# Optimization experiments

Hardware: AMD Instinct MI355X
Metric: run time of the kernel (lower is better)

## Reference

```python
import jax, jax.numpy as jnp
import numpy as np

EPS = 1e-5
TOP_K = 50

def _layernorm(h, g, b):
    mu = jnp.mean(h, axis=-1, keepdims=True)
    var = jnp.mean((h - mu) ** 2, axis=-1, keepdims=True)
    return (h - mu) * jax.lax.rsqrt(var + EPS) * g + b

def setup_inputs() -> dict:
    key = jax.random.key(0)
    ks = jax.random.split(key, 8)
    B, D, E = 16384, 384, 2048
    return {
        "x": jax.random.normal(ks[0], (B, D), jnp.float32),
        "We": jax.random.normal(ks[1], (D, E), jnp.float32) * 0.05,
        "be": jax.random.normal(ks[2], (E,), jnp.float32) * 0.01,
        "g1": jnp.ones((E,), jnp.float32),
        "b1": jnp.zeros((E,), jnp.float32),
        "Wd": jax.random.normal(ks[3], (E, D), jnp.float32) * 0.02,
        "bd": jax.random.normal(ks[4], (D,), jnp.float32) * 0.01,
        "Wb": jax.random.normal(ks[5], (E, D), jnp.float32) * 0.02,
        "bb": jax.random.normal(ks[6], (D,), jnp.float32) * 0.01,
        "g2": jnp.ones((D,), jnp.float32),
        "b2": jnp.zeros((D,), jnp.float32),
    }

def reference(x, We, be, g1, b1, Wd, bd, Wb, bb, g2, b2):
    # encoder: Linear -> LayerNorm -> ReLU
    h = jax.nn.relu(_layernorm(x @ We + be, g1, b1))  # [B, E]
    # top-k sparsification: zero all but top-50 per row (scatter mask, matches torch)
    _, idx = jax.lax.top_k(h, TOP_K)                  # [B, K]
    rows = jnp.arange(h.shape[0])[:, None]
    mask = jnp.zeros_like(h).at[rows, idx].set(1.0)
    sparse = h * mask                                 # [B, E]
    recon = sparse @ Wd + bd                          # [B, D]
    separated = _layernorm(sparse @ Wb + bb, g2, b2)  # [B, D]
    return recon, sparse, separated
```

## Files before the change

kernel.cpp:

```cpp
#include <hip/hip_runtime.h>
#include <hip/hip_bf16.h>
#include <stdint.h>

#define B_D   384
#define B_E   2048
#define TOPK  50
#define LN_EPS 1e-5f
#define NKS   18
#define NKP   12
#define FIX_WINDOW 2e-4f

typedef short bf16x8 __attribute__((ext_vector_type(8)));
typedef float f32x4  __attribute__((ext_vector_type(4)));

__device__ __forceinline__ float wave_sum_f(float v) {
#pragma unroll
    for (int d = 1; d < 64; d <<= 1) v += __shfl_xor(v, d, 64);
    return v;
}
__device__ __forceinline__ int wave_sum_i(int v) {
#pragma unroll
    for (int d = 1; d < 64; d <<= 1) v += __shfl_xor(v, d, 64);
    return v;
}
__device__ __forceinline__ float wave_max_f(float v) {
#pragma unroll
    for (int d = 1; d < 64; d <<= 1) v = fmaxf(v, __shfl_xor(v, d, 64));
    return v;
}

__device__ __forceinline__ ushort f2bf_hi(float v) {
    __hip_bfloat16 b = __float2bfloat16(v);
    return *(ushort*)&b;
}
__device__ __forceinline__ ushort f2bf_lo(float v) {
    __hip_bfloat16 b = __float2bfloat16(v);
    float rem = v - __bfloat162float(b);
    __hip_bfloat16 l = __float2bfloat16(rem);
    return *(ushort*)&l;
}

__device__ __forceinline__ void llds16(const void* g, void* l) {
    __builtin_amdgcn_global_load_lds((const __attribute__((address_space(1))) void*)g,
                                     (__attribute__((address_space(3))) void*)l, 16, 0, 0);
}

__global__ __launch_bounds__(256) void pack_A(const float* __restrict__ x, ushort* __restrict__ Ap,
                                              int* __restrict__ cntr)
{
    const int ks = blockIdx.x, mt = blockIdx.y, t = threadIdx.x;
    if (cntr && t == 0 && ks == 0 && mt == 0) *cntr = 0;
#pragma unroll
    for (int q = 0; q < 8; ++q) {
        const int s = q * 256 + t;
        const int m = s & 255, kg = s >> 8;
        const int kp = ks * 64 + kg * 8;
        const int hi = (kp < 384);
        const int ksrc = hi ? kp : kp - 384;
        const float* src = x + (size_t)(mt * 256 + m) * B_D + ksrc;
        float4 v0 = *(const float4*)src;
        float4 v1 = *(const float4*)(src + 4);
        float vv[8] = {v0.x, v0.y, v0.z, v0.w, v1.x, v1.y, v1.z, v1.w};
        ushort o[8];
#pragma unroll
        for (int e = 0; e < 8; ++e)
            o[e] = hi ? f2bf_hi(vv[e]) : f2bf_lo(vv[e]);
        *(uint4*)(Ap + ((size_t)(mt * NKP + ks) * 2048 + s) * 8) = *(uint4*)o;
    }
}

__global__ __launch_bounds__(256) void pack_B(const float* __restrict__ We, ushort* __restrict__ Bp)
{
    const int ks = blockIdx.x, nt = blockIdx.y, t = threadIdx.x;
#pragma unroll
    for (int q = 0; q < 8; ++q) {
        const int s = q * 256 + t;
        const int nl = s & 255, kg = s >> 8;
        const int kp = ks * 64 + kg * 8;
        const int hi = (kp < 384);
        const int ksrc = hi ? kp : kp - 384;
        const int ng = nt * 256 + nl;
        ushort o[8];
#pragma unroll
        for (int e = 0; e < 8; ++e) {
            float v = We[(size_t)(ksrc + e) * B_E + ng];
            o[e] = hi ? f2bf_hi(v) : f2bf_lo(v);
        }
        *(uint4*)(Bp + ((size_t)(nt * NKP + ks) * 2048 + s) * 8) = *(uint4*)o;
    }
}

__global__ __launch_bounds__(128) void pack_W(
    const float* __restrict__ Wd, const float* __restrict__ Wb, uint* __restrict__ Wp)
{
    const int e = blockIdx.x, t = threadIdx.x;
#pragma unroll
    for (int j = 0; j < 3; ++j) {
        const int c = t + 128 * j;
        const ushort d = f2bf_hi(Wd[(size_t)e * B_D + c]);
        const ushort b = f2bf_hi(Wb[(size_t)e * B_D + c]);
        Wp[(size_t)e * B_D + c] = ((uint)b << 16) | (uint)d;
    }
}

__global__ __launch_bounds__(512, 2) void enc_mfma256(
    const ushort* __restrict__ Ap, const ushort* __restrict__ Bp,
    const float* __restrict__ be, float* __restrict__ y)
{
    __shared__ __align__(16) ushort As[2][16384];
    __shared__ __align__(16) ushort Bs[2][16384];
    const int t = threadIdx.x, lane = t & 63, w = t >> 6;
    const int wr = w >> 2, wc = w & 3;
    const int gid = blockIdx.x;
    const int swz = (gid & 7) * 64 + (gid >> 3);
    const int nt = swz & 7, mt = swz >> 3;
    const ushort* gA = Ap + (size_t)mt * NKP * 16384;
    const ushort* gB = Bp + (size_t)nt * NKP * 16384;

    f32x4 acc[8][4];
#pragma unroll
    for (int i = 0; i < 8; ++i)
#pragma unroll
        for (int j = 0; j < 4; ++j)
#pragma unroll
            for (int r = 0; r < 4; ++r) acc[i][j][r] = 0.f;

    const int l15 = lane & 15, l4 = lane >> 4;

#define STAGE256(ls_, buf_)                                                     \
    {                                                                           \
        const int lsv = (ls_);                                                  \
        const int ksA = (lsv < 6) ? lsv : lsv - 6;                              \
        const int ksB = (lsv < 12) ? lsv : lsv - 12;                            \
        const ushort* a_src = gA + (size_t)ksA * 16384 + t * 8;                 \
        const ushort* b_src = gB + (size_t)ksB * 16384 + t * 8;                 \
        _Pragma("unroll")                                                       \
        for (int q = 0; q < 4; ++q) {                                           \
            llds16(a_src + q * 4096, &As[buf_][t * 8 + q * 4096]);              \
            llds16(b_src + q * 4096, &Bs[buf_][t * 8 + q * 4096]);              \
        }                                                                       \
    }

    STAGE256(0, 0);
    __syncthreads();

    for (int ls = 0; ls < NKS; ++ls) {
        const int cur = ls & 1;
        if (ls + 1 < NKS) STAGE256(ls + 1, cur ^ 1);
#pragma unroll
        for (int ko = 0; ko < 2; ++ko) {
            const int kg = ko * 4 + l4;
            bf16x8 af[8], bfr[4];
#pragma unroll
            for (int i = 0; i < 8; ++i)
                af[i] = *(const bf16x8*)&As[cur][(kg * 256 + wr * 128 + i * 16 + l15) * 8];
#pragma unroll
            for (int j = 0; j < 4; ++j)
                bfr[j] = *(const bf16x8*)&Bs[cur][(kg * 256 + wc * 64 + j * 16 + l15) * 8];
#pragma unroll
            for (int i = 0; i < 8; ++i)
#pragma unroll
                for (int j = 0; j < 4; ++j)
                    acc[i][j] = __builtin_amdgcn_mfma_f32_16x16x32_bf16(af[i], bfr[j], acc[i][j], 0, 0, 0);
        }
        if (ls + 1 < NKS) __syncthreads();
    }
#undef STAGE256

    float bev[4];
#pragma unroll
    for (int j = 0; j < 4; ++j) bev[j] = be[nt * 256 + wc * 64 + j * 16 + l15];
#pragma unroll
    for (int i = 0; i < 8; ++i)
#pragma unroll
        for (int j = 0; j < 4; ++j)
#pragma unroll
            for (int r = 0; r < 4; ++r) {
                const int row = mt * 256 + wr * 128 + i * 16 + l4 * 4 + r;
                const int col = nt * 256 + wc * 64 + j * 16 + l15;
                y[(size_t)row * B_E + col] = acc[i][j][r] + bev[j];
            }
}

__global__ __launch_bounds__(256) void enc_gemm_f32(
    const float* __restrict__ x, const float* __restrict__ We,
    const float* __restrict__ be, float* __restrict__ y)
{
    __shared__ float As[8][128];
    __shared__ float Bs[8][128];
    const int t  = threadIdx.x;
    const int m0 = blockIdx.y * 128;
    const int n0 = blockIdx.x * 128;
    const int tx = t & 15, ty = t >> 4;
    const int la_m = t >> 1, la_k = (t & 1) * 4;
    const int lb_k = t >> 5, lb_c = (t & 31) * 4;

    float acc[8][8];
#pragma unroll
    for (int i = 0; i < 8; ++i)
#pragma unroll
        for (int j = 0; j < 8; ++j) acc[i][j] = 0.f;

    for (int k0 = 0; k0 < B_D; k0 += 8) {
        float4 a = *(const float4*)&x[(size_t)(m0 + la_m) * B_D + k0 + la_k];
        float4 b = *(const float4*)&We[(size_t)(k0 + lb_k) * B_E + n0 + lb_c];
        __syncthreads();
        As[la_k + 0][la_m] = a.x;
        As[la_k + 1][la_m] = a.y;
        As[la_k + 2][la_m] = a.z;
        As[la_k + 3][la_m] = a.w;
        *(float4*)&Bs[lb_k][lb_c] = b;
        __syncthreads();
#pragma unroll
        for (int kk = 0; kk < 8; ++kk) {
            float4 a0 = *(const float4*)&As[kk][ty * 4];
            float4 a1 = *(const float4*)&As[kk][ty * 4 + 64];
            float4 b0 = *(const float4*)&Bs[kk][tx * 4];
            float4 b1 = *(const float4*)&Bs[kk][tx * 4 + 64];
            float av[8] = {a0.x,a0.y,a0.z,a0.w,a1.x,a1.y,a1.z,a1.w};
            float bv[8] = {b0.x,b0.y,b0.z,b0.w,b1.x,b1.y,b1.z,b1.w};
#pragma unroll
            for (int i = 0; i < 8; ++i)
#pragma unroll
                for (int j = 0; j < 8; ++j)
                    acc[i][j] = fmaf(av[i], bv[j], acc[i][j]);
        }
    }
    float4 beL = *(const float4*)&be[n0 + tx * 4];
    float4 beH = *(const float4*)&be[n0 + 64 + tx * 4];
    float bl[8] = {beL.x,beL.y,beL.z,beL.w,beH.x,beH.y,beH.z,beH.w};
#pragma unroll
    for (int i = 0; i < 8; ++i) {
        int row = m0 + ty * 4 + (i & 3) + (i >> 2) * 64;
        float4 o0 = {acc[i][0]+bl[0], acc[i][1]+bl[1], acc[i][2]+bl[2], acc[i][3]+bl[3]};
        float4 o1 = {acc[i][4]+bl[4], acc[i][5]+bl[5], acc[i][6]+bl[6], acc[i][7]+bl[7]};
        *(float4*)&y[(size_t)row * B_E + n0 + tx * 4]      = o0;
        *(float4*)&y[(size_t)row * B_E + n0 + 64 + tx * 4] = o1;
    }
}

__device__ __forceinline__ int ln_topk_row(
    float (&h)[32], int lane, const float* __restrict__ g1, const float* __restrict__ b1,
    float* __restrict__ row, int* __restrict__ IwR, float* __restrict__ VwR,
    float* __restrict__ ldsv, int* __restrict__ ldsi)
{
    float s = 0.f;
#pragma unroll
    for (int j = 0; j < 32; ++j) s += h[j];
    s = wave_sum_f(s);
    const float mu = s * (1.f / B_E);
    float ss = 0.f;
#pragma unroll
    for (int j = 0; j < 32; ++j) { float d = h[j] - mu; ss += d * d; }
    ss = wave_sum_f(ss);
    const float rstd = rsqrtf(ss * (1.f / B_E) + LN_EPS);
#pragma unroll
    for (int q = 0; q < 8; ++q) {
        float4 g  = *(const float4*)&g1[q * 256 + lane * 4];
        float4 bb = *(const float4*)&b1[q * 256 + lane * 4];
        float gg[4]  = {g.x,g.y,g.z,g.w};
        float bbv[4] = {bb.x,bb.y,bb.z,bb.w};
#pragma unroll
        for (int i = 0; i < 4; ++i) {
            int j = q*4+i;
            h[j] = fmaxf(fmaf((h[j] - mu) * rstd, gg[i], bbv[i]), 0.f);
        }
    }
    float mx = h[0];
#pragma unroll
    for (int j = 1; j < 32; ++j) mx = fmaxf(mx, h[j]);
    mx = wave_max_f(mx);

    float vlo = 0.f, vhi = __uint_as_float(__float_as_uint(mx) + 1u);
    int cl = 2048;
    bool window = false;
    for (int it = 0; it < 20; ++it) {
        float mid = 0.5f * (vlo + vhi);
        if (it == 0 && 2.2f > vlo && 2.2f < vhi) mid = 2.2f;
        if (!(mid > vlo && mid < vhi)) break;
        int c = 0;
#pragma unroll
        for (int j = 0; j < 32; ++j)
            c += (int)__popcll(__ballot(h[j] >= mid));
        if (c >= TOPK) { vlo = mid; cl = c; if (c <= 64) { window = true; break; } }
        else vhi = mid;
    }
    unsigned lo = __float_as_uint(vlo);
    if (!window) {
        unsigned hi = __float_as_uint(vhi);
        while (hi - lo > 1u) {
            const unsigned mid = lo + ((hi - lo) >> 1);
            const float mf = __uint_as_float(mid);
            int c = 0;
#pragma unroll
            for (int j = 0; j < 32; ++j)
                c += (int)__popcll(__ballot(h[j] >= mf));
            if (c >= TOPK) { lo = mid; cl = c; if (c <= 64) break; }
            else hi = mid;
        }
    }
    const float T0 = __uint_as_float(lo);

    unsigned selmask = 0u;
    int flag = 0;
    bool fastSel = (cl <= 64 && T0 > 0.f);

    if (fastSel) {
        ldsv[lane] = -1.f;
        ldsi[lane] = 1 << 20;
        asm volatile("s_waitcnt lgkmcnt(0)" ::: "memory");
        int base = 0;
#pragma unroll
        for (int j = 0; j < 32; ++j) {
            const bool p = (h[j] >= T0);
            const unsigned long long m = __ballot(p);
            if (p) {
                const int pos = base + (int)__popcll(m & ((1ull << lane) - 1ull));
                ldsv[pos] = h[j];
                ldsi[pos] = (j >> 2) * 256 + lane * 4 + (j & 3);
            }
            base += (int)__popcll(m);
        }
        asm volatile("s_waitcnt lgkmcnt(0)" ::: "memory");
        float sv = ldsv[lane];
        int   si = ldsi[lane];
#pragma unroll
        for (int k = 2; k <= 64; k <<= 1) {
#pragma unroll
            for (int jj = k >> 1; jj > 0; jj >>= 1) {
                const float ov = __shfl_xor(sv, jj, 64);
                const int   oi = __shfl_xor(si, jj, 64);
                const bool dirUp = ((lane & k) == 0);
                const bool lower = ((lane & jj) == 0);
                const bool mineBefore = (sv > ov) || (sv == ov && si < oi);
                const bool keep = (lower == dirUp) ? mineBefore : !mineBefore;
                if (!keep) { sv = ov; si = oi; }
            }
        }
        const float T    = __shfl(sv, TOPK - 1, 64);
        const int   idxT = __shfl(si, TOPK - 1, 64);
        float v51;
        if (cl > TOPK) {
            v51 = __shfl(sv, TOPK, 64);
        } else {
            float bb = -1.f;
#pragma unroll
            for (int j = 0; j < 32; ++j) bb = (h[j] < T0) ? fmaxf(bb, h[j]) : bb;
            v51 = wave_max_f(bb);
        }
        flag = (T - v51 < FIX_WINDOW) ? 1 : 0;
#pragma unroll
        for (int j = 0; j < 32; ++j) {
            const int e = (j >> 2) * 256 + lane * 4 + (j & 3);
            if (h[j] > T || (h[j] == T && e <= idxT)) selmask |= (1u << j);
        }
        if (lane < TOPK) { IwR[lane] = si; VwR[lane] = sv; }
    } else {
        const float T = T0;
        int cgt = 0, ceq = 0;
        float below = -1.f;
#pragma unroll
        for (int j = 0; j < 32; ++j) {
            cgt += (h[j] > T); ceq += (h[j] == T);
            if (h[j] < T) below = fmaxf(below, h[j]);
        }
        const int cgt_t = wave_sum_i(cgt);
        const int ceq_t = wave_sum_i(ceq);
        below = wave_max_f(below);
        const int need = TOPK - cgt_t;

        if (cgt_t + ceq_t == TOPK) {
#pragma unroll
            for (int j = 0; j < 32; ++j) if (h[j] >= T) selmask |= (1u << j);
        } else {
            int base = 0;
            for (int q = 0; q < 8; ++q) {
                int tc = 0;
#pragma unroll
                for (int i = 0; i < 4; ++i) tc += (h[q*4+i] == T);
                int ip = tc;
#pragma unroll
                for (int d = 1; d < 64; d <<= 1) {
                    int o = __shfl_up(ip, d, 64);
                    if (lane >= d) ip += o;
                }
                int rk  = base + ip - tc;
                int tot = __shfl(ip, 63, 64);
#pragma unroll
                for (int i = 0; i < 4; ++i) {
                    int j = q*4+i;
                    if (h[j] > T) selmask |= (1u << j);
                    else if (h[j] == T) { if (rk < need) selmask |= (1u << j); rk++; }
                }
                base += tot;
            }
        }
        if (T > 0.f) {
            if (cgt_t + ceq_t != TOPK && ceq_t > need) flag = 1;
            else if (T - below < FIX_WINDOW) flag = 1;
        }
        const int myc = __popc(selmask);
        int ip = myc;
#pragma unroll
        for (int d = 1; d < 64; d <<= 1) {
            int o = __shfl_up(ip, d, 64);
            if (lane >= d) ip += o;
        }
        int pos = ip - myc;
        for (int j = 0; j < 32; ++j) {
            if ((selmask >> j) & 1u) {
                int e = (j >> 2) * 256 + lane * 4 + (j & 3);
                IwR[pos] = e;
                VwR[pos] = h[j];
                pos++;
            }
        }
    }

#pragma unroll
    for (int q = 0; q < 8; ++q) {
        float4 o;
        o.x = ((selmask >> (q*4+0)) & 1u) ? h[q*4+0] : 0.f;
        o.y = ((selmask >> (q*4+1)) & 1u) ? h[q*4+1] : 0.f;
        o.z = ((selmask >> (q*4+2)) & 1u) ? h[q*4+2] : 0.f;
        o.w = ((selmask >> (q*4+3)) & 1u) ? h[q*4+3] : 0.f;
        *(float4*)&row[q * 256 + lane * 4] = o;
    }
    return flag;
}

__global__ __launch_bounds__(256) void ln_relu_topk_k(
    float* __restrict__ y, const float* __restrict__ g1, const float* __restrict__ b1,
    int* __restrict__ Iw, float* __restrict__ Vw,
    int* __restrict__ flags, int* __restrict__ rowlist, int* __restrict__ cntr)
{
    __shared__ float ldsv[4][64];
    __shared__ int   ldsi[4][64];
    const int lane = threadIdx.x & 63;
    const int w = threadIdx.x >> 6;
    const int r = blockIdx.x * 4 + w;
    float* row = y + (size_t)r * B_E;
    float h[32];
#pragma unroll
    for (int q = 0; q < 8; ++q) {
        float4 v = *(const float4*)&row[q * 256 + lane * 4];
        h[q*4+0] = v.x; h[q*4+1] = v.y; h[q*4+2] = v.z; h[q*4+3] = v.w;
    }
    int flag = ln_topk_row(h, lane, g1, b1, row, Iw + r * TOPK, Vw + r * TOPK,
                           ldsv[w], ldsi[w]);
    if (flags && lane == 0) {
        flags[r] = flag;
        if (flag) {
            int p = atomicAdd(cntr, 1);
            rowlist[p] = r;
        }
    }
}

__global__ __launch_bounds__(256) void fixup_recompute(
    const float* __restrict__ x, const float* __restrict__ We, const float* __restrict__ be,
    float* __restrict__ y, const int* __restrict__ rowlist, const int* __restrict__ cntr)
{
    const int nflag = *cntr;
    const int rb = blockIdx.y * 8;
    if (rb >= nflag) return;
    const int nact = min(nflag - rb, 8);
    const int t = threadIdx.x;

    __shared__ float xs[8][B_D];
    __shared__ int   rIdx[8];
    if (t < 8) rIdx[t] = (t < nact) ? rowlist[rb + t] : -1;
    __syncthreads();
#pragma unroll
    for (int i = 0; i < 8; ++i) {
        if (i < nact) {
            const float* src = x + (size_t)rIdx[i] * B_D;
            for (int j = t; j < B_D; j += 256) xs[i][j] = src[j];
        } else {
            for (int j = t; j < B_D; j += 256) xs[i][j] = 0.f;
        }
    }
    __syncthreads();

    const int c = blockIdx.x * 256 + t;
    const float bc = be[c];
    float acc[8];
#pragma unroll
    for (int i = 0; i < 8; ++i) acc[i] = bc;
#pragma unroll 4
    for (int k = 0; k < B_D; ++k) {
        const float w = We[(size_t)k * B_E + c];
#pragma unroll
        for (int i = 0; i < 8; ++i) acc[i] = fmaf(xs[i][k], w, acc[i]);
    }
#pragma unroll
    for (int i = 0; i < 8; ++i)
        if (i < nact) y[(size_t)rIdx[i] * B_E + c] = acc[i];
}

__global__ __launch_bounds__(256) void fixup_select(
    float* __restrict__ y, const float* __restrict__ g1, const float* __restrict__ b1,
    int* __restrict__ Iw, float* __restrict__ Vw, const int* __restrict__ flags)
{
    __shared__ float ldsv[4][64];
    __shared__ int   ldsi[4][64];
    const int w = threadIdx.x >> 6;
    const int r = blockIdx.x * 4 + w;
    if (!flags[r]) return;
    const int lane = threadIdx.x & 63;
    float* row = y + (size_t)r * B_E;
    float h[32];
#pragma unroll
    for (int q = 0; q < 8; ++q) {
        float4 v = *(const float4*)&row[q * 256 + lane * 4];
        h[q*4+0] = v.x; h[q*4+1] = v.y; h[q*4+2] = v.z; h[q*4+3] = v.w;
    }
    ln_topk_row(h, lane, g1, b1, row, Iw + r * TOPK, Vw + r * TOPK,
                ldsv[w], ldsi[w]);
}

__global__ __launch_bounds__(128) void decode_packed(
    const int* __restrict__ Iw, const float* __restrict__ Vw,
    const uint* __restrict__ Wp, const float* __restrict__ bd,
    const float* __restrict__ bbias, const float* __restrict__ g2,
    const float* __restrict__ b2, float* __restrict__ recon, float* __restrict__ sep)
{
    __shared__ int   sI[TOPK];
    __shared__ float sV[TOPK];
    __shared__ float red[2];
    const int r = blockIdx.x, t = threadIdx.x;
    if (t < TOPK) { sI[t] = Iw[r * TOPK + t]; sV[t] = Vw[r * TOPK + t]; }
    __syncthreads();
    float ad[3], ab[3];
#pragma unroll
    for (int j = 0; j < 3; ++j) { ad[j] = bd[t + 128*j]; ab[j] = bbias[t + 128*j]; }
#pragma unroll 2
    for (int i = 0; i < TOPK; ++i) {
        const int   idx = sI[i];
        const float v   = sV[i];
        const uint* wp  = Wp + (size_t)idx * B_D;
#pragma unroll
        for (int j = 0; j < 3; ++j) {
            const uint u = wp[t + 128*j];
            const float wd = __uint_as_float(u << 16);
            const float wb = __uint_as_float(u & 0xFFFF0000u);
            ad[j] = fmaf(v, wd, ad[j]);
            ab[j] = fmaf(v, wb, ab[j]);
        }
    }
#pragma unroll
    for (int j = 0; j < 3; ++j) recon[(size_t)r * B_D + t + 128*j] = ad[j];
    float s = ab[0] + ab[1] + ab[2];
    s = wave_sum_f(s);
    if ((t & 63) == 0) red[t >> 6] = s;
    __syncthreads();
    const float mu = (red[0] + red[1]) * (1.f / B_D);
    __syncthreads();
    float ss = 0.f;
#pragma unroll
    for (int j = 0; j < 3; ++j) { float d = ab[j] - mu; ss += d * d; }
    ss = wave_sum_f(ss);
    if ((t & 63) == 0) red[t >> 6] = ss;
    __syncthreads();
    const float rstd = rsqrtf((red[0] + red[1]) * (1.f / B_D) + LN_EPS);
#pragma unroll
    for (int j = 0; j < 3; ++j) {
        int c = t + 128*j;
        sep[(size_t)r * B_D + c] = fmaf((ab[j] - mu) * rstd, g2[c], b2[c]);
    }
}

__global__ __launch_bounds__(128) void decode_f32(
    const int* __restrict__ Iw, const float* __restrict__ Vw,
    const float* __restrict__ Wd, const float* __restrict__ bd,
    const float* __restrict__ Wb, const float* __restrict__ bbias,
    const float* __restrict__ g2, const float* __restrict__ b2,
    float* __restrict__ recon, float* __restrict__ sep)
{
    __shared__ int   sI[TOPK];
    __shared__ float sV[TOPK];
    __shared__ float red[2];
    const int r = blockIdx.x, t = threadIdx.x;
    if (t < TOPK) { sI[t] = Iw[r * TOPK + t]; sV[t] = Vw[r * TOPK + t]; }
    __syncthreads();
    float ad[3], ab[3];
#pragma unroll
    for (int j = 0; j < 3; ++j) { ad[j] = bd[t + 128*j]; ab[j] = bbias[t + 128*j]; }
#pragma unroll 2
    for (int i = 0; i < TOPK; ++i) {
        const int   idx = sI[i];
        const float v   = sV[i];
        const float* wd = Wd + (size_t)idx * B_D;
        const float* wb = Wb + (size_t)idx * B_D;
#pragma unroll
        for (int j = 0; j < 3; ++j) {
            ad[j] = fmaf(v, wd[t + 128*j], ad[j]);
            ab[j] = fmaf(v, wb[t + 128*j], ab[j]);
        }
    }
#pragma unroll
    for (int j = 0; j < 3; ++j) recon[(size_t)r * B_D + t + 128*j] = ad[j];
    float s = ab[0] + ab[1] + ab[2];
    s = wave_sum_f(s);
    if ((t & 63) == 0) red[t >> 6] = s;
    __syncthreads();
    const float mu = (red[0] + red[1]) * (1.f / B_D);
    __syncthreads();
    float ss = 0.f;
#pragma unroll
    for (int j = 0; j < 3; ++j) { float d = ab[j] - mu; ss += d * d; }
    ss = wave_sum_f(ss);
    if ((t & 63) == 0) red[t >> 6] = ss;
    __syncthreads();
    const float rstd = rsqrtf((red[0] + red[1]) * (1.f / B_D) + LN_EPS);
#pragma unroll
    for (int j = 0; j < 3; ++j) {
        int c = t + 128*j;
        sep[(size_t)r * B_D + c] = fmaf((ab[j] - mu) * rstd, g2[c], b2[c]);
    }
}

extern "C" void kernel_launch(void* const* d_in, const int* in_sizes, int n_in,
                              void* d_out, int out_size, void* d_ws, size_t ws_size,
                              hipStream_t stream)
{
    const float* x  = (const float*)d_in[0];
    const float* We = (const float*)d_in[1];
    const float* be = (const float*)d_in[2];
    const float* g1 = (const float*)d_in[3];
    const float* b1 = (const float*)d_in[4];
    const float* Wd = (const float*)d_in[5];
    const float* bd = (const float*)d_in[6];
    const float* Wb = (const float*)d_in[7];
    const float* bb = (const float*)d_in[8];
    const float* g2 = (const float*)d_in[9];
    const float* b2 = (const float*)d_in[10];

    const int Brows = in_sizes[0] / B_D;
    float* recon  = (float*)d_out;
    float* sparse = recon + (size_t)Brows * B_D;
    float* sep    = sparse + (size_t)Brows * B_E;

    char* ws = (char*)d_ws;
    int*   Iw      = (int*)ws;
    float* Vw      = (float*)(ws + 3276800);
    int*   flags   = (int*)(ws + 6553600);
    int*   rowlist = (int*)(ws + 6619136);
    int*   cntr    = (int*)(ws + 6684672);
    const size_t apOff = 6688768;
    const size_t bpOff = apOff + (size_t)64 * NKP * 2048 * 16;
    const size_t need  = bpOff + (size_t)8 * NKP * 2048 * 16;

    if (ws_size >= need) {
        ushort* Ap = (ushort*)(ws + apOff);
        ushort* Bp = (ushort*)(ws + bpOff);
        uint*   Wp = (uint*)(ws + apOff);
        pack_A<<<dim3(NKP, 64), dim3(256), 0, stream>>>(x, Ap, cntr);
        pack_B<<<dim3(NKP, 8),  dim3(256), 0, stream>>>(We, Bp);
        enc_mfma256<<<dim3(512), dim3(512), 0, stream>>>(Ap, Bp, be, sparse);
        pack_W<<<dim3(B_E), dim3(128), 0, stream>>>(Wd, Wb, Wp);
        ln_relu_topk_k<<<dim3(Brows / 4), dim3(256), 0, stream>>>(sparse, g1, b1, Iw, Vw, flags, rowlist, cntr);
        fixup_recompute<<<dim3(8, Brows / 8), dim3(256), 0, stream>>>(x, We, be, sparse, rowlist, cntr);
        fixup_select<<<dim3(Brows / 4), dim3(256), 0, stream>>>(sparse, g1, b1, Iw, Vw, flags);
        decode_packed<<<dim3(Brows), dim3(128), 0, stream>>>(Iw, Vw, Wp, bd, bb, g2, b2, recon, sep);
    } else {
        enc_gemm_f32<<<dim3(16, 128), dim3(256), 0, stream>>>(x, We, be, sparse);
        ln_relu_topk_k<<<dim3(Brows / 4), dim3(256), 0, stream>>>(sparse, g1, b1, Iw, Vw, nullptr, nullptr, nullptr);
        decode_f32<<<dim3(Brows), dim3(128), 0, stream>>>(Iw, Vw, Wd, bd, Wb, bb, g2, b2, recon, sep);
    }
}
```

Baseline: 287.7 us.

## Merge packing kernels and fuse fixup recompute with reselection into one persistent kernel

Combines pack_A and pack_B into a single launch and folds the Wd/Wb bf16 packing into the top-k kernel as extra blocks. The separate fixup_recompute and fixup_select kernels become one persistent fixup kernel. It recomputes flagged rows in fp32 into shared memory and reruns LN/top-k directly, removing the per-row flags array and the full-grid select pass. This cuts launch count and removes the wide grid of mostly-idle fixup blocks, at the cost of a 128-block fixup kernel with heavy shared-memory and register use.

New measurement: 332.1 us. 1.15x slower.

```diff
diff --git a/kernel.cpp b/kernel.cpp
--- a/kernel.cpp
+++ b/kernel.cpp
@@ -45,61 +45,49 @@
                                      (__attribute__((address_space(3))) void*)l, 16, 0, 0);
 }
 
-__global__ __launch_bounds__(256) void pack_A(const float* __restrict__ x, ushort* __restrict__ Ap,
-                                              int* __restrict__ cntr)
-{
-    const int ks = blockIdx.x, mt = blockIdx.y, t = threadIdx.x;
-    if (cntr && t == 0 && ks == 0 && mt == 0) *cntr = 0;
-#pragma unroll
-    for (int q = 0; q < 8; ++q) {
-        const int s = q * 256 + t;
-        const int m = s & 255, kg = s >> 8;
-        const int kp = ks * 64 + kg * 8;
-        const int hi = (kp < 384);
-        const int ksrc = hi ? kp : kp - 384;
-        const float* src = x + (size_t)(mt * 256 + m) * B_D + ksrc;
-        float4 v0 = *(const float4*)src;
-        float4 v1 = *(const float4*)(src + 4);
-        float vv[8] = {v0.x, v0.y, v0.z, v0.w, v1.x, v1.y, v1.z, v1.w};
-        ushort o[8];
-#pragma unroll
-        for (int e = 0; e < 8; ++e)
-            o[e] = hi ? f2bf_hi(vv[e]) : f2bf_lo(vv[e]);
-        *(uint4*)(Ap + ((size_t)(mt * NKP + ks) * 2048 + s) * 8) = *(uint4*)o;
-    }
-}
-
-__global__ __launch_bounds__(256) void pack_B(const float* __restrict__ We, ushort* __restrict__ Bp)
-{
-    const int ks = blockIdx.x, nt = blockIdx.y, t = threadIdx.x;
-#pragma unroll
-    for (int q = 0; q < 8; ++q) {
-        const int s = q * 256 + t;
-        const int nl = s & 255, kg = s >> 8;
-        const int kp = ks * 64 + kg * 8;
-        const int hi = (kp < 384);
-        const int ksrc = hi ? kp : kp - 384;
-        const int ng = nt * 256 + nl;
-        ushort o[8];
-#pragma unroll
-        for (int e = 0; e < 8; ++e) {
-            float v = We[(size_t)(ksrc + e) * B_E + ng];
-            o[e] = hi ? f2bf_hi(v) : f2bf_lo(v);
-        }
-        *(uint4*)(Bp + ((size_t)(nt * NKP + ks) * 2048 + s) * 8) = *(uint4*)o;
-    }
-}
-
-__global__ __launch_bounds__(128) void pack_W(
-    const float* __restrict__ Wd, const float* __restrict__ Wb, uint* __restrict__ Wp)
-{
-    const int e = blockIdx.x, t = threadIdx.x;
-#pragma unroll
-    for (int j = 0; j < 3; ++j) {
-        const int c = t + 128 * j;
-        const ushort d = f2bf_hi(Wd[(size_t)e * B_D + c]);
-        const ushort b = f2bf_hi(Wb[(size_t)e * B_D + c]);
-        Wp[(size_t)e * B_D + c] = ((uint)b << 16) | (uint)d;
+__global__ __launch_bounds__(256) void pack_AB(
+    const float* __restrict__ x, const float* __restrict__ We,
+    ushort* __restrict__ Ap, ushort* __restrict__ Bp, int* __restrict__ cntr)
+{
+    const int ks = blockIdx.x, yb = blockIdx.y, t = threadIdx.x;
+    if (cntr && t == 0 && ks == 0 && yb == 0) *cntr = 0;
+    if (yb < 64) {
+        const int mt = yb;
+#pragma unroll
+        for (int q = 0; q < 8; ++q) {
+            const int s = q * 256 + t;
+            const int m = s & 255, kg = s >> 8;
+            const int kp = ks * 64 + kg * 8;
+            const int hi = (kp < 384);
+            const int ksrc = hi ? kp : kp - 384;
+            const float* src = x + (size_t)(mt * 256 + m) * B_D + ksrc;
+            float4 v0 = *(const float4*)src;
+            float4 v1 = *(const float4*)(src + 4);
+            float vv[8] = {v0.x, v0.y, v0.z, v0.w, v1.x, v1.y, v1.z, v1.w};
+            ushort o[8];
+#pragma unroll
+            for (int e = 0; e < 8; ++e)
+                o[e] = hi ? f2bf_hi(vv[e]) : f2bf_lo(vv[e]);
+            *(uint4*)(Ap + ((size_t)(mt * NKP + ks) * 2048 + s) * 8) = *(uint4*)o;
+        }
+    } else {
+        const int nt = yb - 64;
+#pragma unroll
+        for (int q = 0; q < 8; ++q) {
+            const int s = q * 256 + t;
+            const int nl = s & 255, kg = s >> 8;
+            const int kp = ks * 64 + kg * 8;
+            const int hi = (kp < 384);
+            const int ksrc = hi ? kp : kp - 384;
+            const int ng = nt * 256 + nl;
+            ushort o[8];
+#pragma unroll
+            for (int e = 0; e < 8; ++e) {
+                float v = We[(size_t)(ksrc + e) * B_E + ng];
+                o[e] = hi ? f2bf_hi(v) : f2bf_lo(v);
+            }
+            *(uint4*)(Bp + ((size_t)(nt * NKP + ks) * 2048 + s) * 8) = *(uint4*)o;
+        }
     }
 }
 
@@ -429,10 +417,223 @@
     return flag;
 }
 
-__global__ __launch_bounds__(256) void ln_relu_topk_k(
+__global__ __launch_bounds__(256) void topk_packW(
     float* __restrict__ y, const float* __restrict__ g1, const float* __restrict__ b1,
     int* __restrict__ Iw, float* __restrict__ Vw,
-    int* __restrict__ flags, int* __restrict__ rowlist, int* __restrict__ cntr)
+    int* __restrict__ rowlist, int* __restrict__ cntr,
+    const float* __restrict__ Wd, const float* __restrict__ Wb, uint* __restrict__ Wp,
+    int nTopk)
+{
+    __shared__ float ldsv[4][64];
+    __shared__ int   ldsi[4][64];
+    const int bid = blockIdx.x;
+    const int t = threadIdx.x;
+    if (bid >= nTopk) {
+        const int e = (bid - nTopk) * 2 + (t >> 7);
+        const int tt = t & 127;
+#pragma unroll
+        for (int j = 0; j < 3; ++j) {
+            const int c = tt + 128 * j;
+            const ushort d = f2bf_hi(Wd[(size_t)e * B_D + c]);
+            const ushort b = f2bf_hi(Wb[(size_t)e * B_D + c]);
+            Wp[(size_t)e * B_D + c] = ((uint)b << 16) | (uint)d;
+        }
+        return;
+    }
+    const int lane = t & 63;
+    const int w = t >> 6;
+    const int r = bid * 4 + w;
+    float* row = y + (size_t)r * B_E;
+    float h[32];
+#pragma unroll
+    for (int q = 0; q < 8; ++q) {
+        float4 v = *(const float4*)&row[q * 256 + lane * 4];
+        h[q*4+0] = v.x; h[q*4+1] = v.y; h[q*4+2] = v.z; h[q*4+3] = v.w;
+    }
+    int flag = ln_topk_row(h, lane, g1, b1, row, Iw + r * TOPK, Vw + r * TOPK,
+                           ldsv[w], ldsi[w]);
+    if (rowlist && lane == 0 && flag) {
+        int p = atomicAdd(cntr, 1);
+        rowlist[p] = r;
+    }
+}
+
+__global__ __launch_bounds__(256) void fixup_fused(
+    const float* __restrict__ x, const float* __restrict__ We, const float* __restrict__ be,
+    const float* __restrict__ g1, const float* __restrict__ b1,
+    float* __restrict__ y, int* __restrict__ Iw, float* __restrict__ Vw,
+    const int* __restrict__ rowlist, const int* __restrict__ cntr)
+{
+    const int nflag = *cntr;
+    __shared__ float xs[8][B_D];
+    __shared__ float hy[8][B_E];
+    __shared__ float ldsv[4][64];
+    __shared__ int   ldsi[4][64];
+    __shared__ int   rIdx[8];
+    const int t = threadIdx.x;
+    const int w = t >> 6, lane = t & 63;
+
+    for (int rb = blockIdx.x * 8; rb < nflag; rb += gridDim.x * 8) {
+        const int nact = min(nflag - rb, 8);
+        __syncthreads();
+        if (t < 8) rIdx[t] = (t < nact) ? rowlist[rb + t] : -1;
+        __syncthreads();
+#pragma unroll
+        for (int i = 0; i < 8; ++i) {
+            if (i < nact) {
+                const float* src = x + (size_t)rIdx[i] * B_D;
+                for (int j = t; j < B_D; j += 256) xs[i][j] = src[j];
+            } else {
+                for (int j = t; j < B_D; j += 256) xs[i][j] = 0.f;
+            }
+        }
+        __syncthreads();
+
+        float bev[8];
+#pragma unroll
+        for (int jj = 0; jj < 8; ++jj) bev[jj] = be[t + 256 * jj];
+        float acc[8][8];
+#pragma unroll
+        for (int i = 0; i < 8; ++i)
+#pragma unroll
+            for (int jj = 0; jj < 8; ++jj) acc[i][jj] = bev[jj];
+#pragma unroll 2
+        for (int k = 0; k < B_D; ++k) {
+            const float* wr = We + (size_t)k * B_E;
+            float w8[8];
+#pragma unroll
+            for (int jj = 0; jj < 8; ++jj) w8[jj] = wr[t + 256 * jj];
+#pragma unroll
+            for (int i = 0; i < 8; ++i) {
+                const float xv = xs[i][k];
+#pragma unroll
+                for (int jj = 0; jj < 8; ++jj) acc[i][jj] = fmaf(xv, w8[jj], acc[i][jj]);
+            }
+        }
+#pragma unroll
+        for (int i = 0; i < 8; ++i)
+#pragma unroll
+            for (int jj = 0; jj < 8; ++jj) hy[i][t + 256 * jj] = acc[i][jj];
+        __syncthreads();
+
+        for (int ii = w; ii < nact; ii += 4) {
+            const int r = rIdx[ii];
+            float h[32];
+#pragma unroll
+            for (int q = 0; q < 8; ++q) {
+                float4 v = *(const float4*)&hy[ii][q * 256 + lane * 4];
+                h[q*4+0] = v.x; h[q*4+1] = v.y; h[q*4+2] = v.z; h[q*4+3] = v.w;
+            }
+            ln_topk_row(h, lane, g1, b1, y + (size_t)r * B_E,
+                        Iw + r * TOPK, Vw + r * TOPK, ldsv[w], ldsi[w]);
+        }
+    }
+}
+
+__global__ __launch_bounds__(128) void decode_packed(
+    const int* __restrict__ Iw, const float* __restrict__ Vw,
+    const uint* __restrict__ Wp, const float* __restrict__ bd,
+    const float* __restrict__ bbias, const float* __restrict__ g2,
+    const float* __restrict__ b2, float* __restrict__ recon, float* __restrict__ sep)
+{
+    __shared__ int   sI[TOPK];
+    __shared__ float sV[TOPK];
+    __shared__ float red[2];
+    const int r = blockIdx.x, t = threadIdx.x;
+    if (t < TOPK) { sI[t] = Iw[r * TOPK + t]; sV[t] = Vw[r * TOPK + t]; }
+    __syncthreads();
+    float ad[3], ab[3];
+#pragma unroll
+    for (int j = 0; j < 3; ++j) { ad[j] = bd[t + 128*j]; ab[j] = bbias[t + 128*j]; }
+#pragma unroll 2
+    for (int i = 0; i < TOPK; ++i) {
+        const int   idx = sI[i];
+        const float v   = sV[i];
+        const uint* wp  = Wp + (size_t)idx * B_D;
+#pragma unroll
+        for (int j = 0; j < 3; ++j) {
+            const uint u = wp[t + 128*j];
+            const float wd = __uint_as_float(u << 16);
+            const float wb = __uint_as_float(u & 0xFFFF0000u);
+            ad[j] = fmaf(v, wd, ad[j]);
+            ab[j] = fmaf(v, wb, ab[j]);
+        }
+    }
+#pragma unroll
+    for (int j = 0; j < 3; ++j) recon[(size_t)r * B_D + t + 128*j] = ad[j];
+    float s = ab[0] + ab[1] + ab[2];
+    s = wave_sum_f(s);
+    if ((t & 63) == 0) red[t >> 6] = s;
+    __syncthreads();
+    const float mu = (red[0] + red[1]) * (1.f / B_D);
+    __syncthreads();
+    float ss = 0.f;
+#pragma unroll
+    for (int j = 0; j < 3; ++j) { float d = ab[j] - mu; ss += d * d; }
+    ss = wave_sum_f(ss);
+    if ((t & 63) == 0) red[t >> 6] = ss;
+    __syncthreads();
+    const float rstd = rsqrtf((red[0] + red[1]) * (1.f / B_D) + LN_EPS);
+#pragma unroll
+    for (int j = 0; j < 3; ++j) {
+        int c = t + 128*j;
+        sep[(size_t)r * B_D + c] = fmaf((ab[j] - mu) * rstd, g2[c], b2[c]);
+    }
+}
+
+__global__ __launch_bounds__(128) void decode_f32(
+    const int* __restrict__ Iw, const float* __restrict__ Vw,
+    const float* __restrict__ Wd, const float* __restrict__ bd,
+    const float* __restrict__ Wb, const float* __restrict__ bbias,
+    const float* __restrict__ g2, const float* __restrict__ b2,
+    float* __restrict__ recon, float* __restrict__ sep)
+{
+    __shared__ int   sI[TOPK];
+    __shared__ float sV[TOPK];
+    __shared__ float red[2];
+    const int r = blockIdx.x, t = threadIdx.x;
+    if (t < TOPK) { sI[t] = Iw[r * TOPK + t]; sV[t] = Vw[r * TOPK + t]; }
+    __syncthreads();
+    float ad[3], ab[3];
+#pragma unroll
+    for (int j = 0; j < 3; ++j) { ad[j] = bd[t + 128*j]; ab[j] = bbias[t + 128*j]; }
+#pragma unroll 2
+    for (int i = 0; i < TOPK; ++i) {
+        const int   idx = sI[i];
+        const float v   = sV[i];
+        const float* wd = Wd + (size_t)idx * B_D;
+        const float* wb = Wb + (size_t)idx * B_D;
+#pragma unroll
+        for (int j = 0; j < 3; ++j) {
+            ad[j] = fmaf(v, wd[t + 128*j], ad[j]);
+            ab[j] = fmaf(v, wb[t + 128*j], ab[j]);
+        }
+    }
+#pragma unroll
+    for (int j = 0; j < 3; ++j) recon[(size_t)r * B_D + t + 128*j] = ad[j];
+    float s = ab[0] + ab[1] + ab[2];
+    s = wave_sum_f(s);
+    if ((t & 63) == 0) red[t >> 6] = s;
+    __syncthreads();
+    const float mu = (red[0] + red[1]) * (1.f / B_D);
+    __syncthreads();
+    float ss = 0.f;
+#pragma unroll
+    for (int j = 0; j < 3; ++j) { float d = ab[j] - mu; ss += d * d; }
+    ss = wave_sum_f(ss);
+    if ((t & 63) == 0) red[t >> 6] = ss;
+    __syncthreads();
+    const float rstd = rsqrtf((red[0] + red[1]) * (1.f / B_D) + LN_EPS);
+#pragma unroll
+    for (int j = 0; j < 3; ++j) {
+        int c = t + 128*j;
+        sep[(size_t)r * B_D + c] = fmaf((ab[j] - mu) * rstd, g2[c], b2[c]);
+    }
+}
+
+__global__ __launch_bounds__(256) void topk_only(
+    float* __restrict__ y, const float* __restrict__ g1, const float* __restrict__ b1,
+    int* __restrict__ Iw, float* __restrict__ Vw)
 {
     __shared__ float ldsv[4][64];
     __shared__ int   ldsi[4][64];
@@ -446,178 +647,7 @@
         float4 v = *(const float4*)&row[q * 256 + lane * 4];
         h[q*4+0] = v.x; h[q*4+1] = v.y; h[q*4+2] = v.z; h[q*4+3] = v.w;
     }
-    int flag = ln_topk_row(h, lane, g1, b1, row, Iw + r * TOPK, Vw + r * TOPK,
-                           ldsv[w], ldsi[w]);
-    if (flags && lane == 0) {
-        flags[r] = flag;
-        if (flag) {
-            int p = atomicAdd(cntr, 1);
-            rowlist[p] = r;
-        }
-    }
-}
-
-__global__ __launch_bounds__(256) void fixup_recompute(
-    const float* __restrict__ x, const float* __restrict__ We, const float* __restrict__ be,
-    float* __restrict__ y, const int* __restrict__ rowlist, const int* __restrict__ cntr)
-{
-    const int nflag = *cntr;
-    const int rb = blockIdx.y * 8;
-    if (rb >= nflag) return;
-    const int nact = min(nflag - rb, 8);
-    const int t = threadIdx.x;
-
-    __shared__ float xs[8][B_D];
-    __shared__ int   rIdx[8];
-    if (t < 8) rIdx[t] = (t < nact) ? rowlist[rb + t] : -1;
-    __syncthreads();
-#pragma unroll
-    for (int i = 0; i < 8; ++i) {
-        if (i < nact) {
-            const float* src = x + (size_t)rIdx[i] * B_D;
-            for (int j = t; j < B_D; j += 256) xs[i][j] = src[j];
-        } else {
-            for (int j = t; j < B_D; j += 256) xs[i][j] = 0.f;
-        }
-    }
-    __syncthreads();
-
-    const int c = blockIdx.x * 256 + t;
-    const float bc = be[c];
-    float acc[8];
-#pragma unroll
-    for (int i = 0; i < 8; ++i) acc[i] = bc;
-#pragma unroll 4
-    for (int k = 0; k < B_D; ++k) {
-        const float w = We[(size_t)k * B_E + c];
-#pragma unroll
-        for (int i = 0; i < 8; ++i) acc[i] = fmaf(xs[i][k], w, acc[i]);
-    }
-#pragma unroll
-    for (int i = 0; i < 8; ++i)
-        if (i < nact) y[(size_t)rIdx[i] * B_E + c] = acc[i];
-}
-
-__global__ __launch_bounds__(256) void fixup_select(
-    float* __restrict__ y, const float* __restrict__ g1, const float* __restrict__ b1,
-    int* __restrict__ Iw, float* __restrict__ Vw, const int* __restrict__ flags)
-{
-    __shared__ float ldsv[4][64];
-    __shared__ int   ldsi[4][64];
-    const int w = threadIdx.x >> 6;
-    const int r = blockIdx.x * 4 + w;
-    if (!flags[r]) return;
-    const int lane = threadIdx.x & 63;
-    float* row = y + (size_t)r * B_E;
-    float h[32];
-#pragma unroll
-    for (int q = 0; q < 8; ++q) {
-        float4 v = *(const float4*)&row[q * 256 + lane * 4];
-        h[q*4+0] = v.x; h[q*4+1] = v.y; h[q*4+2] = v.z; h[q*4+3] = v.w;
-    }
-    ln_topk_row(h, lane, g1, b1, row, Iw + r * TOPK, Vw + r * TOPK,
-                ldsv[w], ldsi[w]);
-}
-
-__global__ __launch_bounds__(128) void decode_packed(
-    const int* __restrict__ Iw, const float* __restrict__ Vw,
-    const uint* __restrict__ Wp, const float* __restrict__ bd,
-    const float* __restrict__ bbias, const float* __restrict__ g2,
-    const float* __restrict__ b2, float* __restrict__ recon, float* __restrict__ sep)
-{
-    __shared__ int   sI[TOPK];
-    __shared__ float sV[TOPK];
-    __shared__ float red[2];
-    const int r = blockIdx.x, t = threadIdx.x;
-    if (t < TOPK) { sI[t] = Iw[r * TOPK + t]; sV[t] = Vw[r * TOPK + t]; }
-    __syncthreads();
-    float ad[3], ab[3];
-#pragma unroll
-    for (int j = 0; j < 3; ++j) { ad[j] = bd[t + 128*j]; ab[j] = bbias[t + 128*j]; }
-#pragma unroll 2
-    for (int i = 0; i < TOPK; ++i) {
-        const int   idx = sI[i];
-        const float v   = sV[i];
-        const uint* wp  = Wp + (size_t)idx * B_D;
-#pragma unroll
-        for (int j = 0; j < 3; ++j) {
-            const uint u = wp[t + 128*j];
-            const float wd = __uint_as_float(u << 16);
-            const float wb = __uint_as_float(u & 0xFFFF0000u);
-            ad[j] = fmaf(v, wd, ad[j]);
-            ab[j] = fmaf(v, wb, ab[j]);
-        }
-    }
-#pragma unroll
-    for (int j = 0; j < 3; ++j) recon[(size_t)r * B_D + t + 128*j] = ad[j];
-    float s = ab[0] + ab[1] + ab[2];
-    s = wave_sum_f(s);
-    if ((t & 63) == 0) red[t >> 6] = s;
-    __syncthreads();
-    const float mu = (red[0] + red[1]) * (1.f / B_D);
-    __syncthreads();
-    float ss = 0.f;
-#pragma unroll
-    for (int j = 0; j < 3; ++j) { float d = ab[j] - mu; ss += d * d; }
-    ss = wave_sum_f(ss);
-    if ((t & 63) == 0) red[t >> 6] = ss;
-    __syncthreads();
-    const float rstd = rsqrtf((red[0] + red[1]) * (1.f / B_D) + LN_EPS);
-#pragma unroll
-    for (int j = 0; j < 3; ++j) {
-        int c = t + 128*j;
-        sep[(size_t)r * B_D + c] = fmaf((ab[j] - mu) * rstd, g2[c], b2[c]);
-    }
-}
-
-__global__ __launch_bounds__(128) void decode_f32(
-    const int* __restrict__ Iw, const float* __restrict__ Vw,
-    const float* __restrict__ Wd, const float* __restrict__ bd,
-    const float* __restrict__ Wb, const float* __restrict__ bbias,
-    const float* __restrict__ g2, const float* __restrict__ b2,
-    float* __restrict__ recon, float* __restrict__ sep)
-{
-    __shared__ int   sI[TOPK];
-    __shared__ float sV[TOPK];
-    __shared__ float red[2];
-    const int r = blockIdx.x, t = threadIdx.x;
-    if (t < TOPK) { sI[t] = Iw[r * TOPK + t]; sV[t] = Vw[r * TOPK + t]; }
-    __syncthreads();
-    float ad[3], ab[3];
-#pragma unroll
-    for (int j = 0; j < 3; ++j) { ad[j] = bd[t + 128*j]; ab[j] = bbias[t + 128*j]; }
-#pragma unroll 2
-    for (int i = 0; i < TOPK; ++i) {
-        const int   idx = sI[i];
-        const float v   = sV[i];
-        const float* wd = Wd + (size_t)idx * B_D;
-        const float* wb = Wb + (size_t)idx * B_D;
-#pragma unroll
-        for (int j = 0; j < 3; ++j) {
-            ad[j] = fmaf(v, wd[t + 128*j], ad[j]);
-            ab[j] = fmaf(v, wb[t + 128*j], ab[j]);
-        }
-    }
-#pragma unroll
-    for (int j = 0; j < 3; ++j) recon[(size_t)r * B_D + t + 128*j] = ad[j];
-    float s = ab[0] + ab[1] + ab[2];
-    s = wave_sum_f(s);
-    if ((t & 63) == 0) red[t >> 6] = s;
-    __syncthreads();
-    const float mu = (red[0] + red[1]) * (1.f / B_D);
-    __syncthreads();
-    float ss = 0.f;
-#pragma unroll
-    for (int j = 0; j < 3; ++j) { float d = ab[j] - mu; ss += d * d; }
-    ss = wave_sum_f(ss);
-    if ((t & 63) == 0) red[t >> 6] = ss;
-    __syncthreads();
-    const float rstd = rsqrtf((red[0] + red[1]) * (1.f / B_D) + LN_EPS);
-#pragma unroll
-    for (int j = 0; j < 3; ++j) {
-        int c = t + 128*j;
-        sep[(size_t)r * B_D + c] = fmaf((ab[j] - mu) * rstd, g2[c], b2[c]);
-    }
+    ln_topk_row(h, lane, g1, b1, row, Iw + r * TOPK, Vw + r * TOPK, ldsv[w], ldsi[w]);
 }
 
 extern "C" void kernel_launch(void* const* d_in, const int* in_sizes, int n_in,
@@ -644,7 +674,6 @@
     char* ws = (char*)d_ws;
     int*   Iw      = (int*)ws;
     float* Vw      = (float*)(ws + 3276800);
-    int*   flags   = (int*)(ws + 6553600);
     int*   rowlist = (int*)(ws + 6619136);
     int*   cntr    = (int*)(ws + 6684672);
     const size_t apOff = 6688768;
@@ -655,17 +684,16 @@
         ushort* Ap = (ushort*)(ws + apOff);
         ushort* Bp = (ushort*)(ws + bpOff);
         uint*   Wp = (uint*)(ws + apOff);
-        pack_A<<<dim3(NKP, 64), dim3(256), 0, stream>>>(x, Ap, cntr);
-        pack_B<<<dim3(NKP, 8),  dim3(256), 0, stream>>>(We, Bp);
+        pack_AB<<<dim3(NKP, 72), dim3(256), 0, stream>>>(x, We, Ap, Bp, cntr);
         enc_mfma256<<<dim3(512), dim3(512), 0, stream>>>(Ap, Bp, be, sparse);
-        pack_W<<<dim3(B_E), dim3(128), 0, stream>>>(Wd, Wb, Wp);
-        ln_relu_topk_k<<<dim3(Brows / 4), dim3(256), 0, stream>>>(sparse, g1, b1, Iw, Vw, flags, rowlist, cntr);
-        fixup_recompute<<<dim3(8, Brows / 8), dim3(256), 0, stream>>>(x, We, be, sparse, rowlist, cntr);
-        fixup_select<<<dim3(Brows / 4), dim3(256), 0, stream>>>(sparse, g1, b1, Iw, Vw, flags);
+        topk_packW<<<dim3(Brows / 4 + 1024), dim3(256), 0, stream>>>(
+            sparse, g1, b1, Iw, Vw, rowlist, cntr, Wd, Wb, Wp, Brows / 4);
+        fixup_fused<<<dim3(128), dim3(256), 0, stream>>>(
+            x, We, be, g1, b1, sparse, Iw, Vw, rowlist, cntr);
         decode_packed<<<dim3(Brows), dim3(128), 0, stream>>>(Iw, Vw, Wp, bd, bb, g2, b2, recon, sep);
     } else {
         enc_gemm_f32<<<dim3(16, 128), dim3(256), 0, stream>>>(x, We, be, sparse);
-        ln_relu_topk_k<<<dim3(Brows / 4), dim3(256), 0, stream>>>(sparse, g1, b1, Iw, Vw, nullptr, nullptr, nullptr);
+        topk_only<<<dim3(Brows / 4), dim3(256), 0, stream>>>(sparse, g1, b1, Iw, Vw);
         decode_f32<<<dim3(Brows), dim3(128), 0, stream>>>(Iw, Vw, Wd, bd, Wb, bb, g2, b2, recon, sep);
     }
 }
```
